# Kernel tuning notes

Measured on AMD Instinct MI355X. Metric: run time of the kernel, lower is better.

The kernel has to match this reference:

```python
import jax, jax.numpy as jnp
import numpy as np

B0, H0, W0 = 2, 64, 64
C0, E0, N0, R0 = 96, 192, 16, 6


def sass(H, W):
    L = H * W
    o1, o2, o3, o4 = [], [], [], []
    o1i = [-1] * L; o2i = [-1] * L; o3i = [-1] * L; o4i = [-1] * L
    if H % 2 == 1:
        i, j = H - 1, W - 1; jd = 'left'
    else:
        i, j = H - 1, 0; jd = 'right'
    while i > -1:
        idx = i * W + j
        o1i[idx] = len(o1); o1.append(idx)
        if jd == 'right':
            if j < W - 1: j += 1
            else: i -= 1; jd = 'left'
        elif j > 0: j -= 1
        else: i -= 1; jd = 'right'
    i, j = 0, 0; idd = 'down'
    while j < W:
        idx = i * W + j
        o2i[idx] = len(o2); o2.append(idx)
        if idd == 'down':
            if i < H - 1: i += 1
            else: j += 1; idd = 'up'
        elif i > 0: i -= 1
        else: j += 1; idd = 'down'
    for diag in range(H + W - 1):
        for i in range(min(diag + 1, H)):
            j = diag - i
            if j < W:
                idx = i * W + j
                o3i[idx] = len(o3); o3.append(idx)
    for diag in range(H + W - 1):
        for i in range(min(diag + 1, H)):
            j = diag - i
            if j < W:
                idx = i * W + (W - j - 1)
                o4i[idx] = len(o4); o4.append(idx)
    return (o1, o2, o3, o4), (o1i, o2i, o3i, o4i)


def pool_mat(n_in, n_out):
    # adaptive avg pool 1D weighting matrix (torch AdaptiveAvgPool2d semantics)
    P = np.zeros((n_out, n_in), np.float32)
    for i in range(n_out):
        s = (i * n_in) // n_out
        e = -(-((i + 1) * n_in) // n_out)
        P[i, s:e] = 1.0 / (e - s)
    return jnp.asarray(P)


def gconv(x, w, groups, pad):
    return jax.lax.conv_general_dilated(
        x, w, (1, 1), [pad[0], pad[1]],
        dimension_numbers=('NCHW', 'OIHW', 'NCHW'),
        feature_group_count=groups)


def selective_scan(u, delta, A, Bm, Cm, D, delta_bias):
    # u, delta: [B,E,L]; A: [E,N]; Bm, Cm: [B,N,L]; D, delta_bias: [E]
    delta = jax.nn.softplus(delta + delta_bias[None, :, None])
    dA = jnp.exp(jnp.einsum('bel,en->blen', delta, A))          # [B,L,E,N]
    dBu = jnp.einsum('bel,bnl,bel->blen', delta, Bm, u)          # [B,L,E,N]
    def comb(c1, c2):
        a1, b1 = c1; a2, b2 = c2
        return a1 * a2, a2 * b1 + b2
    _, h = jax.lax.associative_scan(comb, (dA, dBu), axis=1)
    return jnp.einsum('blen,bnl->bel', h, Cm) + D[None, :, None] * u


def local_cluster(xc, sim_alpha, sim_beta, f_w, f_b, v_w, v_b, p_w, p_b, w_size=8, K=5):
    Bb, C, H, W = xc.shape
    w, h = H // w_size, W // w_size
    # 'b e (Wg w) (Hg h) -> (b Wg Hg) e w h'
    x = xc.reshape(Bb, C, w_size, w, w_size, h).transpose(0, 2, 4, 1, 3, 5)
    x = x.reshape(Bb * w_size * w_size, C, w, h)
    x1, x2 = jnp.split(x, 2, axis=1)
    f = jnp.einsum('oc,bcwh->bowh', f_w, x1) + f_b[None, :, None, None]
    v = jnp.einsum('oc,bcwh->bowh', v_w, x2) + v_b[None, :, None, None]
    Pw, Ph = pool_mat(w, K), pool_mat(h, K)
    bb, cc = f.shape[0], f.shape[1]
    P = w * h
    cen = jnp.einsum('iw,bcwh,jh->bcij', Pw, f, Ph).reshape(bb, cc, K * K).transpose(0, 2, 1)
    vc = jnp.einsum('iw,bcwh,jh->bcij', Pw, v, Ph).reshape(bb, cc, K * K).transpose(0, 2, 1)
    ff = f.reshape(bb, cc, P).transpose(0, 2, 1)
    nrm = lambda t: t / jnp.maximum(jnp.linalg.norm(t, axis=-1, keepdims=True), 1e-12)
    sim = jax.nn.sigmoid(sim_beta + sim_alpha * jnp.einsum('bkc,bpc->bkp', nrm(cen), nrm(ff)))
    mask = jax.nn.one_hot(jnp.argmax(sim, axis=1), K * K, dtype=sim.dtype).transpose(0, 2, 1)
    sim = sim * mask
    v2 = v.reshape(bb, cc, P).transpose(0, 2, 1)
    agg = (jnp.einsum('bkp,bpc->bkc', sim, v2) + vc) / (sim.sum(-1, keepdims=True) + 1.0)
    out = jnp.einsum('bkc,bkp->bpc', agg, sim)                   # [bb,P,cc]
    out = out.transpose(0, 2, 1).reshape(bb, cc, w, h)
    out = out.reshape(Bb, w_size, w_size, cc, w, h).transpose(0, 3, 1, 4, 2, 5).reshape(Bb, cc, H, W)
    out = jnp.einsum('oc,bchw->bohw', p_w, out) + p_b[None, :, None, None]
    return out.reshape(Bb, C * 0 + p_w.shape[0], H * W)


def _forward(x, conv_h_w, conv_v_w, conv_d1_w, conv_d2_w, fuse_w, in_proj_w, x_proj_w,
             dt_proj_w, dt_proj_b, A_log, D, direction_Bs, out_proj_w,
             sim_alpha, sim_beta, f_w, f_b, v_w, v_b, p_w, p_b,
             cluster_proj_w, cluster_proj_b, branch_channel, ln_w, ln_b, H, W):
    Bt, L, C = x.shape
    E, N = A_log.shape
    R = dt_proj_w.shape[1]
    silu = jax.nn.silu
    x2d = x.reshape(Bt, H, W, C).transpose(0, 3, 1, 2)
    xh = silu(gconv(x2d, conv_h_w, C, ((0, 0), (3, 3))))
    xv = silu(gconv(x2d, conv_v_w, C, ((3, 3), (0, 0))))
    xd1 = silu(gconv(x2d, conv_d1_w, C, ((3, 3), (3, 3))))
    xd2 = silu(gconv(x2d, conv_d2_w, C, ((3, 3), (3, 3))))
    x_conv = jnp.einsum('oc,bchw->bohw', fuse_w, jnp.concatenate([xh, xv, xd1, xd2], 1))
    seq = x_conv.transpose(0, 2, 3, 1).reshape(Bt, L, C)
    xz = seq @ in_proj_w.T
    xp, zp = jnp.split(xz, 2, axis=-1)
    xdbl = xp @ x_proj_w.T
    dt = xdbl[..., :R] @ dt_proj_w.T + dt_proj_b          # bias applied here AND as delta_bias (faithful)
    dt = dt.transpose(0, 2, 1)                            # [B,E,L]
    Bs = xdbl[..., R:R + N].transpose(0, 2, 1)            # [B,N,L]
    Cs = xdbl[..., R + N:].transpose(0, 2, 1)             # [B,N,L]
    A = -jnp.exp(A_log)
    orders, invs = sass(H, W)
    ys = jnp.zeros_like(xp)
    for d in range(4):
        o = jnp.asarray(orders[d], jnp.int32)
        inv = jnp.asarray(invs[d], jnp.int32)
        u = jnp.take(xp, o, axis=1).transpose(0, 2, 1)    # [B,E,L], reordered u only (faithful)
        y = selective_scan(u, dt, A, Bs + direction_Bs[d][None, :, None], Cs, D, dt_proj_b)
        ys = ys + jnp.take(y.transpose(0, 2, 1), inv, axis=1)
    cl = local_cluster(x_conv, sim_alpha, sim_beta, f_w, f_b, v_w, v_b, p_w, p_b)
    cl = cl.transpose(0, 2, 1) @ cluster_proj_w.T + cluster_proj_b
    wch = jax.nn.softmax(branch_channel, axis=0)
    ln = lambda t: (t - t.mean(-1, keepdims=True)) / jnp.sqrt(t.var(-1, keepdims=True) + 1e-5) * ln_w + ln_b
    y = wch[0] * ln(ys) + wch[1] * ln(zp) + wch[2] * ln(cl)
    return y @ out_proj_w.T


def setup_inputs() -> dict:
    key = jax.random.key(0)
    ks = iter(jax.random.split(key, 32))
    def nrm(shape, s=0.02):
        return jax.random.normal(next(ks), shape, jnp.float32) * s
    C, E, N, R = C0, E0, N0, R0
    return {
        'x': jax.random.normal(next(ks), (B0, H0 * W0, C), jnp.float32),
        'H': H0, 'W': W0,
        'conv_h_w': nrm((E, 1, 1, 7), 0.1),
        'conv_v_w': nrm((E, 1, 7, 1), 0.1),
        'conv_d1_w': nrm((E, 1, 7, 7), 0.05),
        'conv_d2_w': nrm((E, 1, 7, 7), 0.05),
        'fuse_w': nrm((C, 4 * E), 0.02),
        'in_proj_w': nrm((2 * E, C), 0.05),
        'x_proj_w': nrm((R + 2 * N, E), 0.05),
        'dt_proj_w': nrm((E, R), 0.1),
        'dt_proj_b': nrm((E,), 1.0) - 4.0,
        'A_log': jnp.log(jnp.tile(jnp.arange(1, N + 1, dtype=jnp.float32)[None, :], (E, 1))),
        'D': jnp.ones((E,), jnp.float32),
        'direction_Bs': nrm((5, N), 0.02),
        'out_proj_w': nrm((C, E), 0.05),
        'sim_alpha': jnp.ones((1,), jnp.float32),
        'sim_beta': jnp.zeros((1,), jnp.float32),
        'f_w': nrm((C // 16, C // 2), 0.1), 'f_b': jnp.zeros((C // 16,), jnp.float32),
        'v_w': nrm((C // 16, C // 2), 0.1), 'v_b': jnp.zeros((C // 16,), jnp.float32),
        'p_w': nrm((C, C // 16), 0.1), 'p_b': jnp.zeros((C,), jnp.float32),
        'cluster_proj_w': nrm((E, C), 0.05), 'cluster_proj_b': jnp.zeros((E,), jnp.float32),
        'branch_channel': jnp.ones((3, E), jnp.float32),
        'ln_w': jnp.ones((E,), jnp.float32), 'ln_b': jnp.zeros((E,), jnp.float32),
    }


def reference(x, H, W, conv_h_w, conv_v_w, conv_d1_w, conv_d2_w, fuse_w, in_proj_w, x_proj_w,
              dt_proj_w, dt_proj_b, A_log, D, direction_Bs, out_proj_w,
              sim_alpha, sim_beta, f_w, f_b, v_w, v_b, p_w, p_b,
              cluster_proj_w, cluster_proj_b, branch_channel, ln_w, ln_b):
    return _forward(x, conv_h_w, conv_v_w, conv_d1_w, conv_d2_w, fuse_w, in_proj_w, x_proj_w,
                    dt_proj_w, dt_proj_b, A_log, D, direction_Bs, out_proj_w,
                    sim_alpha, sim_beta, f_w, f_b, v_w, v_b, p_w, p_b,
                    cluster_proj_w, cluster_proj_b, branch_channel, ln_w, ln_b, H, W)
```

## Files before the change

### kernel.cpp

```cpp
#include <hip/hip_runtime.h>
#include <hip/hip_bf16.h>

#define Bc   2
#define Hc   64
#define Wc   64
#define Lc   4096
#define Cc   96
#define Ec   192
#define Nc   16
#define CATc 768
#define CHUNK 16
#define NCH  256
#define XJ   38

__device__ __forceinline__ int inv_d0(int l) {
    int i = l >> 6, j = l & 63;
    int k = 63 - i;
    int m = (k & 1) ? (63 - j) : j;
    return k * 64 + m;
}
__device__ __forceinline__ int inv_d1(int l) {
    int i = l >> 6, j = l & 63;
    int m = (j & 1) ? (63 - i) : i;
    return j * 64 + m;
}
__device__ __forceinline__ int diag_off(int d) {
    return (d <= 63) ? (d * (d + 1) / 2) : (4096 - (127 - d) * (128 - d) / 2);
}
__device__ __forceinline__ int inv_d2(int l) {
    int i = l >> 6, j = l & 63;
    int d = i + j;
    int st = d > 63 ? d - 63 : 0;
    return diag_off(d) + (i - st);
}
__device__ __forceinline__ int inv_d3(int l) {
    int i = l >> 6, jj = l & 63;
    int j = 63 - jj;
    int d = i + j;
    int st = d > 63 ? d - 63 : 0;
    return diag_off(d) + (i - st);
}

__global__ __launch_bounds__(256) void setup_kernel(
    int* __restrict__ ord, const float* __restrict__ wout,
    float* __restrict__ woutT, const float* __restrict__ fw,
    float* __restrict__ fwT, const float* __restrict__ xw,
    float* __restrict__ xwT) {
    if (blockIdx.x < 16) {
        int l = blockIdx.x * 256 + threadIdx.x;
        ord[0 * Lc + inv_d0(l)] = l;
        ord[1 * Lc + inv_d1(l)] = l;
        ord[2 * Lc + inv_d2(l)] = l;
        ord[3 * Lc + inv_d3(l)] = l;
    } else if (blockIdx.x < 88) {
        int idx = (blockIdx.x - 16) * 256 + threadIdx.x;
        if (idx < Ec * Cc) {
            int k = idx / Cc, o = idx % Cc;
            woutT[idx] = wout[o * Ec + k];
        }
    } else if (blockIdx.x < 376) {
        int idx = (blockIdx.x - 88) * 256 + threadIdx.x;
        int k = idx / Cc, o = idx % Cc;
        fwT[idx] = fw[o * CATc + k];
    } else {
        int idx = (blockIdx.x - 376) * 256 + threadIdx.x;
        if (idx < Ec * XJ) {
            int c = idx / XJ, j = idx % XJ;
            xwT[idx] = xw[j * Ec + c];
        }
    }
}

__global__ __launch_bounds__(256) void transx_kernel(
    const float* __restrict__ x, float* __restrict__ xT) {
    int lt = blockIdx.x, b = blockIdx.y;
    __shared__ float S[64][97];
    const float* src = x + ((size_t)b * Lc + lt * 64) * Cc;
    for (int idx = threadIdx.x; idx < 64 * 96 / 4; idx += 256) {
        int fl = idx * 4;
        int i = fl / 96, c = fl % 96;
        float4 v = *(const float4*)(src + fl);
        S[i][c] = v.x; S[i][c + 1] = v.y; S[i][c + 2] = v.z; S[i][c + 3] = v.w;
    }
    __syncthreads();
    for (int idx = threadIdx.x; idx < 96 * 64; idx += 256) {
        int c = idx >> 6, i = idx & 63;
        xT[((size_t)b * Cc + c) * Lc + lt * 64 + i] = S[i][c];
    }
}

__global__ __launch_bounds__(256) void conv_kernel(
    const float* __restrict__ xT, const float* __restrict__ wh,
    const float* __restrict__ wv, const float* __restrict__ wd1,
    const float* __restrict__ wd2, float* __restrict__ cat) {
    int tile = blockIdx.x, ic = blockIdx.y, b = blockIdx.z;
    int th0 = (tile >> 2) * 16, tw0 = (tile & 3) * 16;
    __shared__ float S[22][24];
    int tid = threadIdx.x;
    const float* xc = xT + ((size_t)b * Cc + ic) * Lc;
    for (int idx = tid; idx < 22 * 22; idx += 256) {
        int r = idx / 22, c = idx % 22;
        int gh = th0 + r - 3, gw = tw0 + c - 3;
        float v = 0.f;
        if (gh >= 0 && gh < 64 && gw >= 0 && gw < 64)
            v = xc[gh * 64 + gw];
        S[r][c] = v;
    }
    __syncthreads();
    int ti = tid >> 4, tj = tid & 15;
    int pix = (th0 + ti) * 64 + (tw0 + tj);
    for (int s = 0; s < 2; s++) {
        int o = 2 * ic + s;
        float ah = 0.f, av = 0.f, a1 = 0.f, a2 = 0.f;
#pragma unroll
        for (int t = 0; t < 7; t++) {
            ah += S[ti + 3][tj + t] * wh[o * 7 + t];
            av += S[ti + t][tj + 3] * wv[o * 7 + t];
        }
#pragma unroll
        for (int r = 0; r < 7; r++)
#pragma unroll
            for (int c2 = 0; c2 < 7; c2++) {
                float sv = S[ti + r][tj + c2];
                a1 += sv * wd1[o * 49 + r * 7 + c2];
                a2 += sv * wd2[o * 49 + r * 7 + c2];
            }
        cat[((size_t)b * CATc + 0 * Ec + o) * Lc + pix] = ah / (1.f + __expf(-ah));
        cat[((size_t)b * CATc + 1 * Ec + o) * Lc + pix] = av / (1.f + __expf(-av));
        cat[((size_t)b * CATc + 2 * Ec + o) * Lc + pix] = a1 / (1.f + __expf(-a1));
        cat[((size_t)b * CATc + 3 * Ec + o) * Lc + pix] = a2 / (1.f + __expf(-a2));
    }
}

__global__ __launch_bounds__(256) void fuse_part(
    const float* __restrict__ cat, const float* __restrict__ fwT,
    float* __restrict__ pxconv) {
    int l  = blockIdx.x * 256 + threadIdx.x;
    int kc = blockIdx.y;
    int b  = blockIdx.z >> 1;
    int o0 = (blockIdx.z & 1) * 48;
    float acc[48];
#pragma unroll
    for (int j = 0; j < 48; j++) acc[j] = 0.f;
    const float* csrc = cat + ((size_t)b * CATc + kc * 96) * Lc + l;
    const float* wsrc = fwT + (size_t)(kc * 96) * Cc + o0;
#pragma unroll 4
    for (int k = 0; k < 96; k++) {
        float v = csrc[(size_t)k * Lc];
        const float* wr = wsrc + (size_t)k * Cc;
#pragma unroll
        for (int j = 0; j < 48; j++) acc[j] += v * wr[j];
    }
    float* dst = pxconv + (((size_t)kc * Bc + b) * Cc + o0) * Lc + l;
#pragma unroll
    for (int j = 0; j < 48; j++) dst[(size_t)j * Lc] = acc[j];
}

__global__ __launch_bounds__(256) void fuse_reduce(
    const float* __restrict__ pxconv, float* __restrict__ xconv) {
    size_t idx = ((size_t)blockIdx.x * 256 + threadIdx.x) * 4;
    const size_t stride = (size_t)Bc * Cc * Lc;
    float4 s = *(const float4*)(pxconv + idx);
#pragma unroll
    for (int k = 1; k < 8; k++) {
        float4 v = *(const float4*)(pxconv + idx + (size_t)k * stride);
        s.x += v.x; s.y += v.y; s.z += v.z; s.w += v.w;
    }
    *(float4*)(xconv + idx) = s;
}

__global__ __launch_bounds__(256) void inproj_kernel(
    const float* __restrict__ xconv, const float* __restrict__ w,
    float* __restrict__ xp, float* __restrict__ zp, float* __restrict__ xpT) {
    int l = blockIdx.x * 256 + threadIdx.x;
    int o0 = blockIdx.y * 8;
    int b = blockIdx.z;
    float acc[8];
#pragma unroll
    for (int j = 0; j < 8; j++) acc[j] = 0.f;
#pragma unroll 4
    for (int c = 0; c < Cc; c += 2) {
        float v0 = xconv[((size_t)b * Cc + c) * Lc + l];
        float v1 = xconv[((size_t)b * Cc + c + 1) * Lc + l];
#pragma unroll
        for (int j = 0; j < 8; j++) {
            acc[j] += v0 * w[(o0 + j) * Cc + c] + v1 * w[(o0 + j) * Cc + c + 1];
        }
    }
#pragma unroll
    for (int j = 0; j < 8; j++) {
        int o = o0 + j;
        if (o < Ec) {
            xp[((size_t)b * Lc + l) * Ec + o] = acc[j];
            xpT[(size_t)o * (Bc * Lc) + b * Lc + l] = acc[j];
        } else {
            zp[((size_t)b * Lc + l) * Ec + (o - Ec)] = acc[j];
        }
    }
}

__global__ __launch_bounds__(256) void xdbl_gemm(
    const float* __restrict__ xpT, const float* __restrict__ xwT,
    float* __restrict__ pxd) {
    int r  = blockIdx.x * 256 + threadIdx.x;
    int kc = blockIdx.y;
    float acc[XJ];
#pragma unroll
    for (int j = 0; j < XJ; j++) acc[j] = 0.f;
    const float* src = xpT + (size_t)(kc * 24) * (Bc * Lc) + r;
    const float* w   = xwT + kc * 24 * XJ;
#pragma unroll 4
    for (int k = 0; k < 24; k++) {
        float v = src[(size_t)k * (Bc * Lc)];
        const float* wr = w + k * XJ;
#pragma unroll
        for (int j = 0; j < XJ; j++) acc[j] += v * wr[j];
    }
    float* dst = pxd + (size_t)kc * XJ * (Bc * Lc) + r;
#pragma unroll
    for (int j = 0; j < XJ; j++) dst[(size_t)j * (Bc * Lc)] = acc[j];
}

__global__ __launch_bounds__(256) void xdbl_reduce(
    const float* __restrict__ pxd, float* __restrict__ dt6R,
    float* __restrict__ BstT, float* __restrict__ CstT) {
    int idx = blockIdx.x * 256 + threadIdx.x;
    float s = 0.f;
#pragma unroll
    for (int kc = 0; kc < 8; kc++) s += pxd[(size_t)kc * XJ * (Bc * Lc) + idx];
    int j = idx >> 13, r = idx & (Bc * Lc - 1);
    int b = r >> 12, l = r & (Lc - 1);
    if (j < 6)       dt6R[j * (Bc * Lc) + r] = s;
    else if (j < 22) BstT[((size_t)b * Nc + (j - 6)) * Lc + l] = s;
    else             CstT[((size_t)b * Nc + (j - 22)) * Lc + l] = s;
}

__global__ __launch_bounds__(192) void delta_kernel(
    const float* __restrict__ dt6R, const float* __restrict__ dtw,
    const float* __restrict__ dtb, float* __restrict__ delta) {
    int r = blockIdx.x;
    int e = threadIdx.x;
    const float* w = dtw + e * 6;
    float s = 2.f * dtb[e];
#pragma unroll
    for (int rr = 0; rr < 6; rr++) s += dt6R[rr * (Bc * Lc) + r] * w[rr];
    delta[(size_t)r * Ec + e] = (s > 20.f) ? s : log1pf(__expf(s));
}


__global__ __launch_bounds__(192, 2) void scan_part1(
    const float* __restrict__ xp, const int* __restrict__ ord,
    const float* __restrict__ delta, const float* __restrict__ BstT,
    const float* __restrict__ A_log, const float* __restrict__ dirB,
    float* __restrict__ hend, float* __restrict__ Pend) {
    int chunk = blockIdx.x, b = blockIdx.y;
    int e = threadIdx.x;
    int l0 = chunk * CHUNK;
    __shared__ int lord[4][CHUNK];
    __shared__ float4 Bs[CHUNK][Nc];
    if (threadIdx.x < 64) {
        int d = threadIdx.x >> 4, t = threadIdx.x & 15;
        lord[d][t] = ord[d * Lc + l0 + t];
    }
    {
        const float* Bb = BstT + (size_t)b * Nc * Lc;
        for (int idx = threadIdx.x; idx < CHUNK * Nc; idx += 192) {
            int n = idx >> 4, t = idx & 15;
            float Bn = Bb[(size_t)n * Lc + l0 + t];
            Bs[t][n] = make_float4(Bn + dirB[0 * Nc + n], Bn + dirB[1 * Nc + n],
                                   Bn + dirB[2 * Nc + n], Bn + dirB[3 * Nc + n]);
        }
    }
    __syncthreads();
    const float* dl  = delta + (size_t)b * Lc * Ec + e;
    const float* xpb = xp + (size_t)b * Lc * Ec + e;
    float de[CHUNK], u0[CHUNK], u1[CHUNK], u2[CHUNK], u3[CHUNK];
#pragma unroll
    for (int t = 0; t < CHUNK; t++) de[t] = dl[(size_t)(l0 + t) * Ec];
#pragma unroll
    for (int t = 0; t < CHUNK; t++) {
        u0[t] = xpb[(size_t)lord[0][t] * Ec];
        u1[t] = xpb[(size_t)lord[1][t] * Ec];
        u2[t] = xpb[(size_t)lord[2][t] * Ec];
        u3[t] = xpb[(size_t)lord[3][t] * Ec];
    }
    float Aen[Nc], P[Nc], h0[Nc], h1[Nc], h2[Nc], h3[Nc];
#pragma unroll
    for (int n = 0; n < Nc; n++) {
        Aen[n] = -__expf(A_log[e * Nc + n]);
        P[n] = 1.f; h0[n] = 0.f; h1[n] = 0.f; h2[n] = 0.f; h3[n] = 0.f;
    }
#pragma unroll
    for (int t = 0; t < CHUNK; t++) {
        float du0 = de[t] * u0[t], du1 = de[t] * u1[t];
        float du2 = de[t] * u2[t], du3 = de[t] * u3[t];
#pragma unroll
        for (int n = 0; n < Nc; n++) {
            float dA = __expf(de[t] * Aen[n]);
            float4 B4 = Bs[t][n];
            P[n] *= dA;
            h0[n] = dA * h0[n] + du0 * B4.x;
            h1[n] = dA * h1[n] + du1 * B4.y;
            h2[n] = dA * h2[n] + du2 * B4.z;
            h3[n] = dA * h3[n] + du3 * B4.w;
        }
    }
    size_t cb = ((size_t)b * NCH + chunk) * 3072 + e;
    const size_t dstr = (size_t)Bc * NCH * 3072;
#pragma unroll
    for (int n = 0; n < Nc; n++) {
        hend[cb + 0 * dstr + n * Ec] = h0[n];
        hend[cb + 1 * dstr + n * Ec] = h1[n];
        hend[cb + 2 * dstr + n * Ec] = h2[n];
        hend[cb + 3 * dstr + n * Ec] = h3[n];
        Pend[cb + n * Ec] = P[n];
    }
}

__global__ __launch_bounds__(64) void scan_mid(
    float* __restrict__ hend, const float* __restrict__ Pend) {
    int blk = blockIdx.x;
    int sub = blk % 48, db = blk / 48;
    int b = db & 1;
    int pair = sub * 64 + threadIdx.x;
    size_t base  = (size_t)db * NCH * 3072 + pair;
    size_t pbase = (size_t)b * NCH * 3072 + pair;
    float h = 0.f;
    float hc = hend[base];
    float P  = Pend[pbase];
    for (int c = 0; c < NCH; c++) {
        float hc_n = 0.f, P_n = 0.f;
        if (c + 1 < NCH) {
            hc_n = hend[base + (size_t)(c + 1) * 3072];
            P_n  = Pend[pbase + (size_t)(c + 1) * 3072];
        }
        hend[base + (size_t)c * 3072] = h;
        h = P * h + hc;
        hc = hc_n; P = P_n;
    }
}

__global__ __launch_bounds__(192, 2) void scan_part2(
    const float* __restrict__ xp, const int* __restrict__ ord,
    const float* __restrict__ delta, const float* __restrict__ BstT,
    const float* __restrict__ CstT, const float* __restrict__ A_log,
    const float* __restrict__ Dp, const float* __restrict__ dirB,
    const float* __restrict__ hend, float* __restrict__ ydir) {
    int chunk = blockIdx.x, b = blockIdx.y;
    int e = threadIdx.x;
    int l0 = chunk * CHUNK;
    __shared__ int lord[4][CHUNK];
    __shared__ float4 Bs[CHUNK][Nc];
    __shared__ float Cs[CHUNK][Nc];
    if (threadIdx.x < 64) {
        int d = threadIdx.x >> 4, t = threadIdx.x & 15;
        lord[d][t] = ord[d * Lc + l0 + t];
    }
    {
        const float* Bb = BstT + (size_t)b * Nc * Lc;
        const float* Cb = CstT + (size_t)b * Nc * Lc;
        for (int idx = threadIdx.x; idx < CHUNK * Nc; idx += 192) {
            int n = idx >> 4, t = idx & 15;
            float Bn = Bb[(size_t)n * Lc + l0 + t];
            Bs[t][n] = make_float4(Bn + dirB[0 * Nc + n], Bn + dirB[1 * Nc + n],
                                   Bn + dirB[2 * Nc + n], Bn + dirB[3 * Nc + n]);
            Cs[t][n] = Cb[(size_t)n * Lc + l0 + t];
        }
    }
    __syncthreads();
    const float* dl  = delta + (size_t)b * Lc * Ec + e;
    const float* xpb = xp + (size_t)b * Lc * Ec + e;
    float de[CHUNK], u0[CHUNK], u1[CHUNK], u2[CHUNK], u3[CHUNK];
#pragma unroll
    for (int t = 0; t < CHUNK; t++) de[t] = dl[(size_t)(l0 + t) * Ec];
#pragma unroll
    for (int t = 0; t < CHUNK; t++) {
        u0[t] = xpb[(size_t)lord[0][t] * Ec];
        u1[t] = xpb[(size_t)lord[1][t] * Ec];
        u2[t] = xpb[(size_t)lord[2][t] * Ec];
        u3[t] = xpb[(size_t)lord[3][t] * Ec];
    }
    float Aen[Nc], h0[Nc], h1[Nc], h2[Nc], h3[Nc];
    size_t cb = ((size_t)b * NCH + chunk) * 3072 + e;
    const size_t dstr = (size_t)Bc * NCH * 3072;
#pragma unroll
    for (int n = 0; n < Nc; n++) {
        Aen[n] = -__expf(A_log[e * Nc + n]);
        h0[n] = hend[cb + 0 * dstr + n * Ec];
        h1[n] = hend[cb + 1 * dstr + n * Ec];
        h2[n] = hend[cb + 2 * dstr + n * Ec];
        h3[n] = hend[cb + 3 * dstr + n * Ec];
    }
    float De = Dp[e];
    float* yo0 = ydir + ((size_t)(0 * Bc + b) * Lc) * Ec + e;
    float* yo1 = ydir + ((size_t)(1 * Bc + b) * Lc) * Ec + e;
    float* yo2 = ydir + ((size_t)(2 * Bc + b) * Lc) * Ec + e;
    float* yo3 = ydir + ((size_t)(3 * Bc + b) * Lc) * Ec + e;
#pragma unroll
    for (int t = 0; t < CHUNK; t++) {
        float du0 = de[t] * u0[t], du1 = de[t] * u1[t];
        float du2 = de[t] * u2[t], du3 = de[t] * u3[t];
        float a0 = De * u0[t], a1 = De * u1[t];
        float a2 = De * u2[t], a3 = De * u3[t];
#pragma unroll
        for (int n = 0; n < Nc; n++) {
            float dA = __expf(de[t] * Aen[n]);
            float4 B4 = Bs[t][n];
            float Cn = Cs[t][n];
            h0[n] = dA * h0[n] + du0 * B4.x;
            h1[n] = dA * h1[n] + du1 * B4.y;
            h2[n] = dA * h2[n] + du2 * B4.z;
            h3[n] = dA * h3[n] + du3 * B4.w;
            a0 += h0[n] * Cn; a1 += h1[n] * Cn;
            a2 += h2[n] * Cn; a3 += h3[n] * Cn;
        }
        int l = l0 + t;
        yo0[(size_t)l * Ec] = a0;
        yo1[(size_t)l * Ec] = a1;
        yo2[(size_t)l * Ec] = a2;
        yo3[(size_t)l * Ec] = a3;
    }
}

__global__ __launch_bounds__(64) void cluster_kernel(
    const float* __restrict__ xconv,
    const float* __restrict__ fwp, const float* __restrict__ fbp,
    const float* __restrict__ vwp, const float* __restrict__ vbp,
    const float* __restrict__ pwp, const float* __restrict__ pbp,
    const float* __restrict__ alphap, const float* __restrict__ betap,
    float* __restrict__ c96) {
    int g = blockIdx.x;
    int b = g >> 6, Wg = (g >> 3) & 7, Hg = g & 7;
    int p = threadIdx.x;
    int wi = p >> 3, hj = p & 7;
    int lsp = (Wg * 8 + wi) * 64 + (Hg * 8 + hj);
    __shared__ float fS[64][6], vS[64][6];
    __shared__ float cen[25][6], vc[25][6], cnorm[25];
    __shared__ float simb[64];
    __shared__ int kb[64];
    __shared__ float agg[25][6];
    float fr[6], vr[6];
#pragma unroll
    for (int oc = 0; oc < 6; oc++) { fr[oc] = fbp[oc]; vr[oc] = vbp[oc]; }
    for (int c = 0; c < 48; c++) {
        float v1 = xconv[((size_t)b * Cc + c) * Lc + lsp];
        float v2 = xconv[((size_t)b * Cc + 48 + c) * Lc + lsp];
#pragma unroll
        for (int oc = 0; oc < 6; oc++) {
            fr[oc] += v1 * fwp[oc * 48 + c];
            vr[oc] += v2 * vwp[oc * 48 + c];
        }
    }
#pragma unroll
    for (int oc = 0; oc < 6; oc++) { fS[p][oc] = fr[oc]; vS[p][oc] = vr[oc]; }
    __syncthreads();
    const int bs[5] = {0, 1, 3, 4, 6}, be[5] = {2, 4, 5, 7, 8};
    for (int t = p; t < 150; t += 64) {
        int k = t / 6, oc = t % 6;
        int ki = k / 5, kj = k % 5;
        float sf = 0.f, sv = 0.f;
        int cnt = 0;
        for (int ii = bs[ki]; ii < be[ki]; ii++)
            for (int jj = bs[kj]; jj < be[kj]; jj++) {
                sf += fS[ii * 8 + jj][oc];
                sv += vS[ii * 8 + jj][oc];
                cnt++;
            }
        cen[k][oc] = sf / cnt;
        vc[k][oc] = sv / cnt;
    }
    __syncthreads();
    if (p < 25) {
        float s = 0.f;
#pragma unroll
        for (int oc = 0; oc < 6; oc++) s += cen[p][oc] * cen[p][oc];
        cnorm[p] = 1.f / fmaxf(sqrtf(s), 1e-12f);
    }
    __syncthreads();
    float fn2 = 0.f;
#pragma unroll
    for (int oc = 0; oc < 6; oc++) fn2 += fr[oc] * fr[oc];
    float finv = 1.f / fmaxf(sqrtf(fn2), 1e-12f);
    float alpha = alphap[0], beta = betap[0];
    float best = -1.f;
    int bestk = 0;
    for (int k = 0; k < 25; k++) {
        float dot = 0.f;
#pragma unroll
        for (int oc = 0; oc < 6; oc++) dot += cen[k][oc] * fr[oc];
        float xv = beta + alpha * dot * cnorm[k] * finv;
        float s = 1.f / (1.f + __expf(-xv));
        if (s > best) { best = s; bestk = k; }
    }
    simb[p] = best;
    kb[p] = bestk;
    __syncthreads();
    if (p < 25) {
        float sum_s = 0.f;
        float av[6];
#pragma unroll
        for (int oc = 0; oc < 6; oc++) av[oc] = vc[p][oc];
        for (int q = 0; q < 64; q++) {
            if (kb[q] == p) {
                float s = simb[q];
                sum_s += s;
#pragma unroll
                for (int oc = 0; oc < 6; oc++) av[oc] += s * vS[q][oc];
            }
        }
        float invd = 1.f / (sum_s + 1.f);
#pragma unroll
        for (int oc = 0; oc < 6; oc++) agg[p][oc] = av[oc] * invd;
    }
    __syncthreads();
    float outp[6];
#pragma unroll
    for (int oc = 0; oc < 6; oc++) outp[oc] = agg[kb[p]][oc] * simb[p];
    float* orow = c96 + ((size_t)b * Lc + lsp) * Cc;
    for (int oo = 0; oo < Cc; oo++) {
        float s = pbp[oo];
#pragma unroll
        for (int oc = 0; oc < 6; oc++) s += outp[oc] * pwp[oo * 6 + oc];
        orow[oo] = s;
    }
}

__global__ __launch_bounds__(256) void clproj_kernel(
    const float* __restrict__ c96, const float* __restrict__ w,
    const float* __restrict__ bias, float* __restrict__ cl) {
    int l = blockIdx.x * 256 + threadIdx.x;
    int o0 = blockIdx.y * 8;
    int b = blockIdx.z;
    const float* row = c96 + ((size_t)b * Lc + l) * Cc;
    float acc[8];
#pragma unroll
    for (int j = 0; j < 8; j++) acc[j] = bias[o0 + j];
#pragma unroll 4
    for (int c = 0; c < Cc; c += 2) {
        float v0 = row[c], v1 = row[c + 1];
#pragma unroll
        for (int j = 0; j < 8; j++) {
            acc[j] += v0 * w[(o0 + j) * Cc + c] + v1 * w[(o0 + j) * Cc + c + 1];
        }
    }
#pragma unroll
    for (int j = 0; j < 8; j++)
        cl[((size_t)b * Lc + l) * Ec + o0 + j] = acc[j];
}

__global__ __launch_bounds__(256) void final_kernel(
    const float* __restrict__ ydir, const float* __restrict__ zp,
    const float* __restrict__ cl, const float* __restrict__ bc,
    const float* __restrict__ lnw, const float* __restrict__ lnb,
    const float* __restrict__ woutT, float* __restrict__ out) {
    __shared__ float comb[4][Ec];
    int wave = threadIdx.x >> 6, lane = threadIdx.x & 63;
    int row = blockIdx.x * 4 + wave;
    int b = row >> 12, lp = row & (Lc - 1);
    int iv0 = inv_d0(lp), iv1 = inv_d1(lp), iv2 = inv_d2(lp), iv3 = inv_d3(lp);
    const float* y0 = ydir + ((size_t)(0 * Bc + b) * Lc + iv0) * Ec;
    const float* y1 = ydir + ((size_t)(1 * Bc + b) * Lc + iv1) * Ec;
    const float* y2 = ydir + ((size_t)(2 * Bc + b) * Lc + iv2) * Ec;
    const float* y3 = ydir + ((size_t)(3 * Bc + b) * Lc + iv3) * Ec;
    const float* zr = zp + ((size_t)b * Lc + lp) * Ec;
    const float* cr = cl + ((size_t)b * Lc + lp) * Ec;
    float ys[3], zv[3], cv[3];
    float s1 = 0, s2 = 0, z1 = 0, z2 = 0, c1 = 0, c2 = 0;
#pragma unroll
    for (int t = 0; t < 3; t++) {
        int i = lane + t * 64;
        float v = y0[i] + y1[i] + y2[i] + y3[i];
        ys[t] = v; s1 += v; s2 += v * v;
        float z = zr[i]; zv[t] = z; z1 += z; z2 += z * z;
        float c = cr[i]; cv[t] = c; c1 += c; c2 += c * c;
    }
#pragma unroll
    for (int o = 32; o >= 1; o >>= 1) {
        s1 += __shfl_xor(s1, o, 64); s2 += __shfl_xor(s2, o, 64);
        z1 += __shfl_xor(z1, o, 64); z2 += __shfl_xor(z2, o, 64);
        c1 += __shfl_xor(c1, o, 64); c2 += __shfl_xor(c2, o, 64);
    }
    const float invE = 1.f / (float)Ec;
    float ym = s1 * invE, yvr = rsqrtf(s2 * invE - ym * ym + 1e-5f);
    float zm = z1 * invE, zvr = rsqrtf(z2 * invE - zm * zm + 1e-5f);
    float cm = c1 * invE, cvr = rsqrtf(c2 * invE - cm * cm + 1e-5f);
#pragma unroll
    for (int t = 0; t < 3; t++) {
        int i = lane + t * 64;
        float g = lnw[i], bb = lnb[i];
        float a0 = (ys[t] - ym) * yvr * g + bb;
        float a1 = (zv[t] - zm) * zvr * g + bb;
        float a2 = (cv[t] - cm) * cvr * g + bb;
        float w0 = bc[i], w1 = bc[Ec + i], w2 = bc[2 * Ec + i];
        float mx = fmaxf(w0, fmaxf(w1, w2));
        float e0 = __expf(w0 - mx), e1 = __expf(w1 - mx), e2 = __expf(w2 - mx);
        float inv = 1.f / (e0 + e1 + e2);
        comb[wave][i] = (e0 * a0 + e1 * a1 + e2 * a2) * inv;
    }
    __syncthreads();
    float r0 = 0.f, r1 = 0.f;
#pragma unroll 4
    for (int k = 0; k < Ec; k++) {
        float cvk = comb[wave][k];
        float w0 = woutT[k * Cc + lane];
        float w1 = woutT[k * Cc + 64 + lane];
        r0 += cvk * w0;
        r1 += cvk * w1;
    }
    float* orow = out + (size_t)row * Cc;
    orow[lane] = r0;
    if (lane < 32) orow[64 + lane] = r1;
}

extern "C" void kernel_launch(void* const* d_in, const int* in_sizes, int n_in,
                              void* d_out, int out_size, void* d_ws, size_t ws_size,
                              hipStream_t stream) {
    const float* x       = (const float*)d_in[0];
    const float* wh      = (const float*)d_in[3];
    const float* wv      = (const float*)d_in[4];
    const float* wd1     = (const float*)d_in[5];
    const float* wd2     = (const float*)d_in[6];
    const float* fw      = (const float*)d_in[7];
    const float* ipw     = (const float*)d_in[8];
    const float* xw      = (const float*)d_in[9];
    const float* dtw     = (const float*)d_in[10];
    const float* dtb     = (const float*)d_in[11];
    const float* A_log   = (const float*)d_in[12];
    const float* Dp      = (const float*)d_in[13];
    const float* dirB    = (const float*)d_in[14];
    const float* wout    = (const float*)d_in[15];
    const float* alphap  = (const float*)d_in[16];
    const float* betap   = (const float*)d_in[17];
    const float* fwp     = (const float*)d_in[18];
    const float* fbp     = (const float*)d_in[19];
    const float* vwp     = (const float*)d_in[20];
    const float* vbp     = (const float*)d_in[21];
    const float* pwp     = (const float*)d_in[22];
    const float* pbp     = (const float*)d_in[23];
    const float* clw     = (const float*)d_in[24];
    const float* clb     = (const float*)d_in[25];
    const float* bc      = (const float*)d_in[26];
    const float* lnw     = (const float*)d_in[27];
    const float* lnb     = (const float*)d_in[28];
    float* out = (float*)d_out;

    float* wsf = (float*)d_ws;
    size_t off = 0;
    int* ord      = (int*)wsf;             off += 4 * Lc;
    float* cat    = wsf + off;             off += (size_t)Bc * CATc * Lc;
    float* xconv  = wsf + off;             off += (size_t)Bc * Cc * Lc;
    float* xp     = wsf + off;             off += (size_t)Bc * Lc * Ec;
    float* zpb    = wsf + off;             off += (size_t)Bc * Lc * Ec;
    float* deltab = wsf + off;             off += (size_t)Bc * Lc * Ec;
    float* BstT   = wsf + off;             off += (size_t)Bc * Lc * Nc;
    float* CstT   = wsf + off;             off += (size_t)Bc * Lc * Nc;
    float* hend   = wsf + off;             off += (size_t)4 * Bc * NCH * Ec * Nc;
    float* Pend   = wsf + off;             off += (size_t)Bc * NCH * Ec * Nc;
    float* woutT  = wsf + off;             off += (size_t)Ec * Cc + 64;
    float* fwT    = wsf + off;             off += (size_t)CATc * Cc;
    float* xwT    = wsf + off;             off += (size_t)Ec * XJ + 64;
    float* xT     = wsf + off;             off += (size_t)Bc * Cc * Lc;
    float* ydir = cat;
    float* c96  = xp;
    float* cl   = deltab;
    float* pxconv = xp;
    float* xpT  = hend;
    float* pxd  = hend + (size_t)Ec * Bc * Lc;
    float* dt6R = pxd + (size_t)8 * XJ * Bc * Lc;

    setup_kernel<<<405, 256, 0, stream>>>(ord, wout, woutT, fw, fwT, xw, xwT);
    transx_kernel<<<dim3(64, 2), 256, 0, stream>>>(x, xT);
    conv_kernel<<<dim3(16, 96, 2), 256, 0, stream>>>(xT, wh, wv, wd1, wd2, cat);
    fuse_part<<<dim3(16, 8, 4), 256, 0, stream>>>(cat, fwT, pxconv);
    fuse_reduce<<<768, 256, 0, stream>>>(pxconv, xconv);
    inproj_kernel<<<dim3(16, 48, 2), 256, 0, stream>>>(xconv, ipw, xp, zpb, xpT);
    xdbl_gemm<<<dim3(32, 8), 256, 0, stream>>>(xpT, xwT, pxd);
    xdbl_reduce<<<1216, 256, 0, stream>>>(pxd, dt6R, BstT, CstT);
    delta_kernel<<<8192, 192, 0, stream>>>(dt6R, dtw, dtb, deltab);
    scan_part1<<<dim3(NCH, 2), 192, 0, stream>>>(xp, ord, deltab, BstT,
                                                 A_log, dirB, hend, Pend);
    scan_mid<<<384, 64, 0, stream>>>(hend, Pend);
    scan_part2<<<dim3(NCH, 2), 192, 0, stream>>>(xp, ord, deltab, BstT, CstT,
                                                 A_log, Dp, dirB, hend, ydir);
    cluster_kernel<<<128, 64, 0, stream>>>(xconv, fwp, fbp, vwp, vbp, pwp, pbp,
                                           alphap, betap, c96);
    clproj_kernel<<<dim3(16, 24, 2), 256, 0, stream>>>(c96, clw, clb, cl);
    final_kernel<<<2048, 256, 0, stream>>>(ydir, zpb, cl, bc, lnw, lnb, woutT, out);
}
```

Measured before the change: 364.0 us.

## Widen in_proj and cluster-proj GEMM tiles with pre-transposed weights and channel-major inputs

The in_proj kernel now computes 48 outputs per thread instead of 8, and the cluster projection computes 24 instead of 8. Both read weights pre-transposed in the setup kernel, so each input channel is a contiguous row. The cluster kernel now writes its output channel-major, so clproj reads inputs coalesced across l instead of striding through rows. This cuts redundant input reads and improves coalescing, at the cost of higher register pressure and fewer blocks. The softplus also switches to fast __logf(1+exp).

```diff
diff --git a/kernel.cpp b/kernel.cpp
--- a/kernel.cpp
+++ b/kernel.cpp
@@ -45,7 +45,9 @@
     int* __restrict__ ord, const float* __restrict__ wout,
     float* __restrict__ woutT, const float* __restrict__ fw,
     float* __restrict__ fwT, const float* __restrict__ xw,
-    float* __restrict__ xwT) {
+    float* __restrict__ xwT, const float* __restrict__ ipw,
+    float* __restrict__ ipwT, const float* __restrict__ clw,
+    float* __restrict__ clwT) {
     if (blockIdx.x < 16) {
         int l = blockIdx.x * 256 + threadIdx.x;
         ord[0 * Lc + inv_d0(l)] = l;
@@ -62,12 +64,20 @@
         int idx = (blockIdx.x - 88) * 256 + threadIdx.x;
         int k = idx / Cc, o = idx % Cc;
         fwT[idx] = fw[o * CATc + k];
-    } else {
+    } else if (blockIdx.x < 405) {
         int idx = (blockIdx.x - 376) * 256 + threadIdx.x;
         if (idx < Ec * XJ) {
             int c = idx / XJ, j = idx % XJ;
             xwT[idx] = xw[j * Ec + c];
         }
+    } else if (blockIdx.x < 549) {
+        int idx = (blockIdx.x - 405) * 256 + threadIdx.x;
+        int c = idx / (2 * Ec), o = idx % (2 * Ec);
+        ipwT[idx] = ipw[o * Cc + c];
+    } else {
+        int idx = (blockIdx.x - 549) * 256 + threadIdx.x;
+        int c = idx / Ec, o = idx % Ec;
+        clwT[idx] = clw[o * Cc + c];
     }
 }
 
@@ -170,32 +180,34 @@
 }
 
 __global__ __launch_bounds__(256) void inproj_kernel(
-    const float* __restrict__ xconv, const float* __restrict__ w,
+    const float* __restrict__ xconv, const float* __restrict__ ipwT,
     float* __restrict__ xp, float* __restrict__ zp, float* __restrict__ xpT) {
     int l = blockIdx.x * 256 + threadIdx.x;
-    int o0 = blockIdx.y * 8;
+    int o0 = blockIdx.y * 48;
     int b = blockIdx.z;
-    float acc[8];
-#pragma unroll
-    for (int j = 0; j < 8; j++) acc[j] = 0.f;
+    float acc[48];
+#pragma unroll
+    for (int j = 0; j < 48; j++) acc[j] = 0.f;
+    const float* csrc = xconv + (size_t)b * Cc * Lc + l;
+    const float* wsrc = ipwT + o0;
 #pragma unroll 4
-    for (int c = 0; c < Cc; c += 2) {
-        float v0 = xconv[((size_t)b * Cc + c) * Lc + l];
-        float v1 = xconv[((size_t)b * Cc + c + 1) * Lc + l];
-#pragma unroll
-        for (int j = 0; j < 8; j++) {
-            acc[j] += v0 * w[(o0 + j) * Cc + c] + v1 * w[(o0 + j) * Cc + c + 1];
-        }
-    }
-#pragma unroll
-    for (int j = 0; j < 8; j++) {
-        int o = o0 + j;
-        if (o < Ec) {
-            xp[((size_t)b * Lc + l) * Ec + o] = acc[j];
-            xpT[(size_t)o * (Bc * Lc) + b * Lc + l] = acc[j];
-        } else {
-            zp[((size_t)b * Lc + l) * Ec + (o - Ec)] = acc[j];
-        }
+    for (int c = 0; c < Cc; c++) {
+        float v = csrc[(size_t)c * Lc];
+        const float* wr = wsrc + c * (2 * Ec);
+#pragma unroll
+        for (int j = 0; j < 48; j++) acc[j] += v * wr[j];
+    }
+    if (o0 < Ec) {
+        float* xr = xp + ((size_t)b * Lc + l) * Ec + o0;
+#pragma unroll
+        for (int j = 0; j < 48; j++) xr[j] = acc[j];
+        float* xt = xpT + (size_t)o0 * (Bc * Lc) + b * Lc + l;
+#pragma unroll
+        for (int j = 0; j < 48; j++) xt[(size_t)j * (Bc * Lc)] = acc[j];
+    } else {
+        float* zr = zp + ((size_t)b * Lc + l) * Ec + (o0 - Ec);
+#pragma unroll
+        for (int j = 0; j < 48; j++) zr[j] = acc[j];
     }
 }
 
@@ -244,7 +256,7 @@
     float s = 2.f * dtb[e];
 #pragma unroll
     for (int rr = 0; rr < 6; rr++) s += dt6R[rr * (Bc * Lc) + r] * w[rr];
-    delta[(size_t)r * Ec + e] = (s > 20.f) ? s : log1pf(__expf(s));
+    delta[(size_t)r * Ec + e] = (s > 20.f) ? s : __logf(1.f + __expf(s));
 }
 
 
@@ -428,7 +440,7 @@
     const float* __restrict__ vwp, const float* __restrict__ vbp,
     const float* __restrict__ pwp, const float* __restrict__ pbp,
     const float* __restrict__ alphap, const float* __restrict__ betap,
-    float* __restrict__ c96) {
+    float* __restrict__ c96T) {
     int g = blockIdx.x;
     int b = g >> 6, Wg = (g >> 3) & 7, Hg = g & 7;
     int p = threadIdx.x;
@@ -516,36 +528,36 @@
     float outp[6];
 #pragma unroll
     for (int oc = 0; oc < 6; oc++) outp[oc] = agg[kb[p]][oc] * simb[p];
-    float* orow = c96 + ((size_t)b * Lc + lsp) * Cc;
+    float* ocol = c96T + (size_t)b * Cc * Lc + lsp;
     for (int oo = 0; oo < Cc; oo++) {
         float s = pbp[oo];
 #pragma unroll
         for (int oc = 0; oc < 6; oc++) s += outp[oc] * pwp[oo * 6 + oc];
-        orow[oo] = s;
+        ocol[(size_t)oo * Lc] = s;
     }
 }
 
 __global__ __launch_bounds__(256) void clproj_kernel(
-    const float* __restrict__ c96, const float* __restrict__ w,
+    const float* __restrict__ c96T, const float* __restrict__ clwT,
     const float* __restrict__ bias, float* __restrict__ cl) {
     int l = blockIdx.x * 256 + threadIdx.x;
-    int o0 = blockIdx.y * 8;
+    int o0 = blockIdx.y * 24;
     int b = blockIdx.z;
-    const float* row = c96 + ((size_t)b * Lc + l) * Cc;
-    float acc[8];
-#pragma unroll
-    for (int j = 0; j < 8; j++) acc[j] = bias[o0 + j];
+    float acc[24];
+#pragma unroll
+    for (int j = 0; j < 24; j++) acc[j] = bias[o0 + j];
+    const float* csrc = c96T + (size_t)b * Cc * Lc + l;
+    const float* wsrc = clwT + o0;
 #pragma unroll 4
-    for (int c = 0; c < Cc; c += 2) {
-        float v0 = row[c], v1 = row[c + 1];
-#pragma unroll
-        for (int j = 0; j < 8; j++) {
-            acc[j] += v0 * w[(o0 + j) * Cc + c] + v1 * w[(o0 + j) * Cc + c + 1];
-        }
-    }
-#pragma unroll
-    for (int j = 0; j < 8; j++)
-        cl[((size_t)b * Lc + l) * Ec + o0 + j] = acc[j];
+    for (int c = 0; c < Cc; c++) {
+        float v = csrc[(size_t)c * Lc];
+        const float* wr = wsrc + c * Ec;
+#pragma unroll
+        for (int j = 0; j < 24; j++) acc[j] += v * wr[j];
+    }
+    float* cr = cl + ((size_t)b * Lc + l) * Ec + o0;
+#pragma unroll
+    for (int j = 0; j < 24; j++) cr[j] = acc[j];
 }
 
 __global__ __launch_bounds__(256) void final_kernel(
@@ -660,20 +672,23 @@
     float* fwT    = wsf + off;             off += (size_t)CATc * Cc;
     float* xwT    = wsf + off;             off += (size_t)Ec * XJ + 64;
     float* xT     = wsf + off;             off += (size_t)Bc * Cc * Lc;
+    float* ipwT   = wsf + off;             off += (size_t)Cc * 2 * Ec;
+    float* clwT   = wsf + off;             off += (size_t)Cc * Ec;
     float* ydir = cat;
-    float* c96  = xp;
+    float* c96T = xp;
     float* cl   = deltab;
     float* pxconv = xp;
     float* xpT  = hend;
     float* pxd  = hend + (size_t)Ec * Bc * Lc;
     float* dt6R = pxd + (size_t)8 * XJ * Bc * Lc;
 
-    setup_kernel<<<405, 256, 0, stream>>>(ord, wout, woutT, fw, fwT, xw, xwT);
+    setup_kernel<<<621, 256, 0, stream>>>(ord, wout, woutT, fw, fwT, xw, xwT,
+                                          ipw, ipwT, clw, clwT);
     transx_kernel<<<dim3(64, 2), 256, 0, stream>>>(x, xT);
     conv_kernel<<<dim3(16, 96, 2), 256, 0, stream>>>(xT, wh, wv, wd1, wd2, cat);
     fuse_part<<<dim3(16, 8, 4), 256, 0, stream>>>(cat, fwT, pxconv);
     fuse_reduce<<<768, 256, 0, stream>>>(pxconv, xconv);
-    inproj_kernel<<<dim3(16, 48, 2), 256, 0, stream>>>(xconv, ipw, xp, zpb, xpT);
+    inproj_kernel<<<dim3(16, 8, 2), 256, 0, stream>>>(xconv, ipwT, xp, zpb, xpT);
     xdbl_gemm<<<dim3(32, 8), 256, 0, stream>>>(xpT, xwT, pxd);
     xdbl_reduce<<<1216, 256, 0, stream>>>(pxd, dt6R, BstT, CstT);
     delta_kernel<<<8192, 192, 0, stream>>>(dt6R, dtw, dtb, deltab);
@@ -683,7 +698,7 @@
     scan_part2<<<dim3(NCH, 2), 192, 0, stream>>>(xp, ord, deltab, BstT, CstT,
                                                  A_log, Dp, dirB, hend, ydir);
     cluster_kernel<<<128, 64, 0, stream>>>(xconv, fwp, fbp, vwp, vbp, pwp, pbp,
-                                           alphap, betap, c96);
-    clproj_kernel<<<dim3(16, 24, 2), 256, 0, stream>>>(c96, clw, clb, cl);
+                                           alphap, betap, c96T);
+    clproj_kernel<<<dim3(16, 8, 2), 256, 0, stream>>>(c96T, clwT, clb, cl);
     final_kernel<<<2048, 256, 0, stream>>>(ydir, zpb, cl, bc, lnw, lnb, woutT, out);
 }
```

After: 367.5 us. Within noise of the previous version (+1.0%).
